# Kernel optimization log

Hardware: AMD Instinct MI355X
Metric: run time of the kernel (lower is better)

## Reference

```python
import jax, jax.numpy as jnp
import numpy as np

H = 16  # num_heads

def setup_inputs() -> dict:
    key = jax.random.key(0)
    ks = jax.random.split(key, 5)
    d = 1024
    s = 0.02
    return {
        'x': jax.random.normal(ks[0], (2, 2048, d), jnp.float32),
        'Wq': jax.random.normal(ks[1], (d, d), jnp.float32) * s,
        'bq': jnp.zeros((d,), jnp.float32),
        'Wk': jax.random.normal(ks[2], (d, d), jnp.float32) * s,
        'bk': jnp.zeros((d,), jnp.float32),
        'Wv': jax.random.normal(ks[3], (d, d), jnp.float32) * s,
        'bv': jnp.zeros((d,), jnp.float32),
        'Wo': jax.random.normal(ks[4], (d, d), jnp.float32) * s,
        'bo': jnp.zeros((d,), jnp.float32),
        'ln_scale': jnp.ones((d,), jnp.float32),
        'ln_bias': jnp.zeros((d,), jnp.float32),
    }

def _layernorm(x, scale, bias, eps=1e-6):
    mu = jnp.mean(x, axis=-1, keepdims=True)
    var = jnp.var(x, axis=-1, keepdims=True)
    return (x - mu) * jax.lax.rsqrt(var + eps) * scale + bias

def reference(x, Wq, bq, Wk, bk, Wv, bv, Wo, bo, ln_scale, ln_bias):
    b, n, d = x.shape
    hd = d // H
    scale = hd ** -0.5
    residual = x
    xn = _layernorm(x, ln_scale, ln_bias)
    # QKV projections, split heads: [b, n, d] -> [b, H, n, hd]
    def split(y):
        return y.reshape(b, n, H, hd).transpose(0, 2, 1, 3)
    q = split(xn @ Wq + bq)
    k = split(xn @ Wk + bk)
    v = split(xn @ Wv + bv)
    attn = jnp.einsum('bhid,bhjd->bhij', q, k) * scale
    attn = jax.nn.softmax(attn, axis=-1)
    out = jnp.einsum('bhij,bhjd->bhid', attn, v)
    out = out.transpose(0, 2, 1, 3).reshape(b, n, d)
    out = out @ Wo + bo
    return out + residual
```

## Files before the change

kernel.cpp:

```cpp
#include <hip/hip_runtime.h>

typedef __bf16 bf16;
typedef __bf16 bf16x8 __attribute__((ext_vector_type(8)));
typedef float f32x4 __attribute__((ext_vector_type(4)));

#define D_MODEL 1024
#define SEQ 2048
#define NH 16
#define HD 64

#define GLD16(gp, lp) __builtin_amdgcn_global_load_lds( \
    (const __attribute__((address_space(1))) void*)(gp), \
    (__attribute__((address_space(3))) void*)(lp), 16, 0, 0)

__device__ __forceinline__ int sigi(int y) {
    return (y & 0x23) | ((y & 0x18) >> 1) | ((y & 0x04) << 2);
}

__global__ __launch_bounds__(256) void ln_kernel(const float* __restrict__ x,
        const float* __restrict__ g, const float* __restrict__ bta,
        bf16* __restrict__ xnb) {
    int tok = blockIdx.x;
    const float* xr = x + (size_t)tok * D_MODEL;
    float v[4];
    float s = 0.f, ss = 0.f;
#pragma unroll
    for (int j = 0; j < 4; ++j) {
        int idx = threadIdx.x + j * 256;
        float t = xr[idx];
        v[j] = t; s += t; ss += t * t;
    }
#pragma unroll
    for (int m = 32; m; m >>= 1) { s += __shfl_xor(s, m, 64); ss += __shfl_xor(ss, m, 64); }
    __shared__ float red_s[4], red_ss[4];
    int w = threadIdx.x >> 6;
    if ((threadIdx.x & 63) == 0) { red_s[w] = s; red_ss[w] = ss; }
    __syncthreads();
    s  = red_s[0] + red_s[1] + red_s[2] + red_s[3];
    ss = red_ss[0] + red_ss[1] + red_ss[2] + red_ss[3];
    float mu  = s * (1.f / D_MODEL);
    float var = ss * (1.f / D_MODEL) - mu * mu;
    float rstd = rsqrtf(var + 1e-6f);
    bf16* orow = xnb + (size_t)tok * D_MODEL;
#pragma unroll
    for (int j = 0; j < 4; ++j) {
        int idx = threadIdx.x + j * 256;
        float xn = (v[j] - mu) * rstd * g[idx] + bta[idx];
        orow[idx] = (bf16)xn;
    }
}

__global__ __launch_bounds__(256) void transpose_kernel(const float* __restrict__ W0,
        const float* __restrict__ W1, const float* __restrict__ W2,
        const float* __restrict__ W3, bf16* __restrict__ wt) {
    __shared__ float tile[32][33];
    int mat = blockIdx.z;
    const float* W = mat == 0 ? W0 : mat == 1 ? W1 : mat == 2 ? W2 : W3;
    bf16* dst = wt + (size_t)mat * D_MODEL * D_MODEL;
    int k0 = blockIdx.x * 32, n0 = blockIdx.y * 32;
    int tx = threadIdx.x & 31, ty0 = threadIdx.x >> 5;
#pragma unroll
    for (int r = 0; r < 4; ++r) {
        int ty = ty0 + r * 8;
        tile[ty][tx] = W[(size_t)(k0 + ty) * D_MODEL + n0 + tx];
    }
    __syncthreads();
#pragma unroll
    for (int r = 0; r < 4; ++r) {
        int ty = ty0 + r * 8;
        dst[(size_t)(n0 + ty) * D_MODEL + k0 + tx] = (bf16)tile[tx][ty];
    }
}

__global__ __launch_bounds__(256) void qkv_gemm(const bf16* __restrict__ A,
        const bf16* __restrict__ Bt, const float* __restrict__ bq,
        const float* __restrict__ bk, const float* __restrict__ bv,
        bf16* __restrict__ qo, bf16* __restrict__ ko, bf16* __restrict__ vto) {
    __shared__ __align__(16) bf16 As[128 * 32];
    __shared__ __align__(16) bf16 Bs[128 * 32];
    int m0 = blockIdx.x * 128, n0 = blockIdx.y * 128;
    int tid = threadIdx.x;
    int w = tid >> 6, l = tid & 63, lm = l & 15, lq = l >> 4;
    int wm = (w >> 1) * 64, wn = (w & 1) * 64;
    f32x4 acc[4][4] = {};
    const bf16* ag = A  + (size_t)(m0 + w * 32 + (l >> 2)) * D_MODEL + (l & 3) * 8;
    const bf16* bg = Bt + (size_t)(n0 + w * 32 + (l >> 2)) * D_MODEL + (l & 3) * 8;
    bf16* asd = &As[(w * 32) * 32];
    bf16* bsd = &Bs[(w * 32) * 32];
    for (int k0 = 0; k0 < D_MODEL; k0 += 32) {
        GLD16(ag,                asd);
        GLD16(ag + 16 * D_MODEL, asd + 16 * 32);
        GLD16(bg,                bsd);
        GLD16(bg + 16 * D_MODEL, bsd + 16 * 32);
        ag += 32; bg += 32;
        __syncthreads();
        bf16x8 af[4], bf_[4];
#pragma unroll
        for (int f = 0; f < 4; ++f) af[f]  = *(const bf16x8*)&As[(wm + f * 16 + lm) * 32 + lq * 8];
#pragma unroll
        for (int f = 0; f < 4; ++f) bf_[f] = *(const bf16x8*)&Bs[(wn + f * 16 + lm) * 32 + lq * 8];
#pragma unroll
        for (int fm = 0; fm < 4; ++fm)
#pragma unroll
            for (int fn = 0; fn < 4; ++fn)
                acc[fm][fn] = __builtin_amdgcn_mfma_f32_16x16x32_bf16(af[fm], bf_[fn], acc[fm][fn], 0, 0, 0);
        __syncthreads();
    }
#pragma unroll
    for (int fn = 0; fn < 4; ++fn) {
        int n_g = n0 + wn + fn * 16 + lm;
        int mat = n_g >> 10, within = n_g & 1023;
        int h = within >> 6, hdp = within & 63;
        float bias = mat == 0 ? bq[within] : mat == 1 ? bk[within] : bv[within];
#pragma unroll
        for (int fm = 0; fm < 4; ++fm) {
#pragma unroll
            for (int r = 0; r < 4; ++r) {
                int m_g = m0 + wm + fm * 16 + lq * 4 + r;
                int b_ = m_g >> 11, i = m_g & 2047;
                int bh = b_ * NH + h;
                float val = acc[fm][fn][r] + bias;
                if (mat == 0) {
                    qo[((size_t)bh * SEQ + i) * HD + hdp] = (bf16)(val * 0.180336888f);
                } else {
                    int jt = i >> 6, jl = i & 63;
                    if (mat == 1) {
                        int idx = sigi(jl);
                        int nt_ = idx >> 4, lm_ = idx & 15;
                        int kc_ = hdp >> 5, lq_ = (hdp >> 3) & 3, e_ = hdp & 7;
                        ko[(size_t)bh * SEQ * HD + (size_t)jt * 4096 +
                           (kc_ * 4 + nt_) * 512 + (lq_ * 16 + lm_) * 8 + e_] = (bf16)val;
                    } else {
                        int nt_ = hdp >> 4, lm_ = hdp & 15;
                        int kc_ = jl >> 5, lq_ = (jl >> 3) & 3, e_ = jl & 7;
                        vto[(size_t)bh * SEQ * HD + (size_t)jt * 4096 +
                            (kc_ * 4 + nt_) * 512 + (lq_ * 16 + lm_) * 8 + e_] = (bf16)val;
                    }
                }
            }
        }
    }
}

__global__ __launch_bounds__(256) void attn_kernel(const bf16* __restrict__ q,
        const bf16* __restrict__ k, const bf16* __restrict__ vt,
        bf16* __restrict__ aout) {
    int i0 = blockIdx.x * 128;
    int bh = blockIdx.y;
    int tid = threadIdx.x;
    int w = tid >> 6, l = tid & 63, lm = l & 15, lq = l >> 4;
    const bf16* qb = q  + (size_t)bh * SEQ * HD;
    const bf16* kp = k  + (size_t)bh * SEQ * HD + l * 8;
    const bf16* vp = vt + (size_t)bh * SEQ * HD + l * 8;

    bf16x8 qf[2][2];
#pragma unroll
    for (int mf = 0; mf < 2; ++mf)
#pragma unroll
        for (int kc = 0; kc < 2; ++kc)
            qf[mf][kc] = *(const bf16x8*)(qb + (size_t)(i0 + w * 32 + mf * 16 + lm) * HD + kc * 32 + lq * 8);

    bf16x8 kcur[2][4];
#pragma unroll
    for (int kc = 0; kc < 2; ++kc)
#pragma unroll
        for (int nt = 0; nt < 4; ++nt)
            kcur[kc][nt] = *(const bf16x8*)(kp + (kc * 4 + nt) * 512);
    kp += 4096;

    f32x4 o[2][4] = {};
    float l_acc[2] = {0.f, 0.f};

    for (int j0 = 0; j0 < SEQ; j0 += 64) {
        bf16x8 vcur[2][4];
#pragma unroll
        for (int kc = 0; kc < 2; ++kc)
#pragma unroll
            for (int nt = 0; nt < 4; ++nt)
                vcur[kc][nt] = *(const bf16x8*)(vp + (kc * 4 + nt) * 512);
        vp += 4096;
        bf16x8 knxt[2][4];
        if (j0 + 64 < SEQ) {
#pragma unroll
            for (int kc = 0; kc < 2; ++kc)
#pragma unroll
                for (int nt = 0; nt < 4; ++nt)
                    knxt[kc][nt] = *(const bf16x8*)(kp + (kc * 4 + nt) * 512);
            kp += 4096;
        }
        f32x4 s[2][4] = {};
#pragma unroll
        for (int kc = 0; kc < 2; ++kc)
#pragma unroll
            for (int nt = 0; nt < 4; ++nt) {
                s[0][nt] = __builtin_amdgcn_mfma_f32_16x16x32_bf16(kcur[kc][nt], qf[0][kc], s[0][nt], 0, 0, 0);
                s[1][nt] = __builtin_amdgcn_mfma_f32_16x16x32_bf16(kcur[kc][nt], qf[1][kc], s[1][nt], 0, 0, 0);
            }
#pragma unroll
        for (int mf = 0; mf < 2; ++mf) {
            float psum = 0.f;
#pragma unroll
            for (int nt = 0; nt < 4; ++nt)
#pragma unroll
                for (int r = 0; r < 4; ++r) {
                    float p = exp2f(s[mf][nt][r]);
                    s[mf][nt][r] = p; psum += p;
                }
            l_acc[mf] += psum;
        }
#pragma unroll
        for (int kc = 0; kc < 2; ++kc) {
            bf16x8 pf[2];
#pragma unroll
            for (int mf = 0; mf < 2; ++mf)
#pragma unroll
                for (int jj = 0; jj < 8; ++jj)
                    pf[mf][jj] = (bf16)s[mf][2 * kc + (jj >> 2)][jj & 3];
#pragma unroll
            for (int nt = 0; nt < 4; ++nt) {
                o[0][nt] = __builtin_amdgcn_mfma_f32_16x16x32_bf16(pf[0], vcur[kc][nt], o[0][nt], 0, 0, 0);
                o[1][nt] = __builtin_amdgcn_mfma_f32_16x16x32_bf16(pf[1], vcur[kc][nt], o[1][nt], 0, 0, 0);
            }
        }
#pragma unroll
        for (int kc = 0; kc < 2; ++kc)
#pragma unroll
            for (int nt = 0; nt < 4; ++nt)
                kcur[kc][nt] = knxt[kc][nt];
    }
    int b_ = bh >> 4, h = bh & 15;
#pragma unroll
    for (int mf = 0; mf < 2; ++mf) {
        l_acc[mf] += __shfl_xor(l_acc[mf], 16, 64);
        l_acc[mf] += __shfl_xor(l_acc[mf], 32, 64);
        float linv[4];
#pragma unroll
        for (int r = 0; r < 4; ++r)
            linv[r] = 1.f / __shfl(l_acc[mf], lq * 4 + r, 64);
#pragma unroll
        for (int nt = 0; nt < 4; ++nt) {
#pragma unroll
            for (int r = 0; r < 4; ++r) {
                int i = i0 + w * 32 + mf * 16 + lq * 4 + r;
                int tok = b_ * SEQ + i;
                aout[(size_t)tok * D_MODEL + h * HD + nt * 16 + lm] = (bf16)(o[mf][nt][r] * linv[r]);
            }
        }
    }
}

__global__ __launch_bounds__(256) void out_gemm(const bf16* __restrict__ A,
        const bf16* __restrict__ Bt, const float* __restrict__ bo,
        const float* __restrict__ resid, float* __restrict__ out) {
    __shared__ __align__(16) bf16 As[128 * 32];
    __shared__ __align__(16) bf16 Bs[128 * 32];
    int m0 = blockIdx.x * 128, n0 = blockIdx.y * 128;
    int tid = threadIdx.x;
    int w = tid >> 6, l = tid & 63, lm = l & 15, lq = l >> 4;
    int wm = (w >> 1) * 64, wn = (w & 1) * 64;
    f32x4 acc[4][4] = {};
    const bf16* ag = A  + (size_t)(m0 + w * 32 + (l >> 2)) * D_MODEL + (l & 3) * 8;
    const bf16* bg = Bt + (size_t)(n0 + w * 32 + (l >> 2)) * D_MODEL + (l & 3) * 8;
    bf16* asd = &As[(w * 32) * 32];
    bf16* bsd = &Bs[(w * 32) * 32];
    for (int k0 = 0; k0 < D_MODEL; k0 += 32) {
        GLD16(ag,                asd);
        GLD16(ag + 16 * D_MODEL, asd + 16 * 32);
        GLD16(bg,                bsd);
        GLD16(bg + 16 * D_MODEL, bsd + 16 * 32);
        ag += 32; bg += 32;
        __syncthreads();
        bf16x8 af[4], bf_[4];
#pragma unroll
        for (int f = 0; f < 4; ++f) af[f]  = *(const bf16x8*)&As[(wm + f * 16 + lm) * 32 + lq * 8];
#pragma unroll
        for (int f = 0; f < 4; ++f) bf_[f] = *(const bf16x8*)&Bs[(wn + f * 16 + lm) * 32 + lq * 8];
#pragma unroll
        for (int fm = 0; fm < 4; ++fm)
#pragma unroll
            for (int fn = 0; fn < 4; ++fn)
                acc[fm][fn] = __builtin_amdgcn_mfma_f32_16x16x32_bf16(af[fm], bf_[fn], acc[fm][fn], 0, 0, 0);
        __syncthreads();
    }
#pragma unroll
    for (int fn = 0; fn < 4; ++fn) {
        int n_g = n0 + wn + fn * 16 + lm;
        float bias = bo[n_g];
#pragma unroll
        for (int fm = 0; fm < 4; ++fm) {
#pragma unroll
            for (int r = 0; r < 4; ++r) {
                int m_g = m0 + wm + fm * 16 + lq * 4 + r;
                size_t idx = (size_t)m_g * D_MODEL + n_g;
                out[idx] = acc[fm][fn][r] + bias + resid[idx];
            }
        }
    }
}

extern "C" void kernel_launch(void* const* d_in, const int* in_sizes, int n_in,
                              void* d_out, int out_size, void* d_ws, size_t ws_size,
                              hipStream_t stream) {
    const float* x  = (const float*)d_in[0];
    const float* Wq = (const float*)d_in[1];
    const float* bq = (const float*)d_in[2];
    const float* Wk = (const float*)d_in[3];
    const float* bk = (const float*)d_in[4];
    const float* Wv = (const float*)d_in[5];
    const float* bv = (const float*)d_in[6];
    const float* Wo = (const float*)d_in[7];
    const float* bo = (const float*)d_in[8];
    const float* g  = (const float*)d_in[9];
    const float* bt = (const float*)d_in[10];
    (void)in_sizes; (void)n_in; (void)out_size; (void)ws_size;

    char* ws = (char*)d_ws;
    const size_t M8 = (size_t)8 << 20;
    bf16* xnb = (bf16*)(ws);
    bf16* wt  = (bf16*)(ws + M8);
    bf16* qb  = (bf16*)(ws + 2 * M8);
    bf16* kb  = (bf16*)(ws + 3 * M8);
    bf16* vtb = (bf16*)(ws + 4 * M8);
    bf16* ao  = xnb;
    float* out = (float*)d_out;

    ln_kernel<<<4096, 256, 0, stream>>>(x, g, bt, xnb);
    transpose_kernel<<<dim3(32, 32, 4), 256, 0, stream>>>(Wq, Wk, Wv, Wo, wt);
    qkv_gemm<<<dim3(32, 24), 256, 0, stream>>>(xnb, wt, bq, bk, bv, qb, kb, vtb);
    attn_kernel<<<dim3(16, 32), 256, 0, stream>>>(qb, kb, vtb, ao);
    out_gemm<<<dim3(32, 8), 256, 0, stream>>>(ao, wt + (size_t)3 * D_MODEL * D_MODEL, bo, x, out);
}
```

Baseline: 233.2 us.

## Use plain K/V-transposed layouts and XCD-aware block mapping in attention

Result: slower. 274.9 us (+17.9%).

```diff
diff --git a/kernel.cpp b/kernel.cpp
--- a/kernel.cpp
+++ b/kernel.cpp
@@ -13,8 +13,8 @@
     (const __attribute__((address_space(1))) void*)(gp), \
     (__attribute__((address_space(3))) void*)(lp), 16, 0, 0)
 
-__device__ __forceinline__ int sigi(int y) {
-    return (y & 0x23) | ((y & 0x18) >> 1) | ((y & 0x04) << 2);
+__device__ __forceinline__ int sigp(int r) {
+    return (r & 0x23) | ((r & 0x0C) << 1) | ((r & 0x10) >> 2);
 }
 
 __global__ __launch_bounds__(256) void ln_kernel(const float* __restrict__ x,
@@ -120,23 +120,9 @@
                 int b_ = m_g >> 11, i = m_g & 2047;
                 int bh = b_ * NH + h;
                 float val = acc[fm][fn][r] + bias;
-                if (mat == 0) {
-                    qo[((size_t)bh * SEQ + i) * HD + hdp] = (bf16)(val * 0.180336888f);
-                } else {
-                    int jt = i >> 6, jl = i & 63;
-                    if (mat == 1) {
-                        int idx = sigi(jl);
-                        int nt_ = idx >> 4, lm_ = idx & 15;
-                        int kc_ = hdp >> 5, lq_ = (hdp >> 3) & 3, e_ = hdp & 7;
-                        ko[(size_t)bh * SEQ * HD + (size_t)jt * 4096 +
-                           (kc_ * 4 + nt_) * 512 + (lq_ * 16 + lm_) * 8 + e_] = (bf16)val;
-                    } else {
-                        int nt_ = hdp >> 4, lm_ = hdp & 15;
-                        int kc_ = jl >> 5, lq_ = (jl >> 3) & 3, e_ = jl & 7;
-                        vto[(size_t)bh * SEQ * HD + (size_t)jt * 4096 +
-                            (kc_ * 4 + nt_) * 512 + (lq_ * 16 + lm_) * 8 + e_] = (bf16)val;
-                    }
-                }
+                if (mat == 0)      qo [((size_t)bh * SEQ + i) * HD + hdp] = (bf16)(val * 0.180336888f);
+                else if (mat == 1) ko [((size_t)bh * SEQ + i) * HD + hdp] = (bf16)val;
+                else               vto[((size_t)bh * HD + hdp) * SEQ + i] = (bf16)val;
             }
         }
     }
@@ -145,13 +131,16 @@
 __global__ __launch_bounds__(256) void attn_kernel(const bf16* __restrict__ q,
         const bf16* __restrict__ k, const bf16* __restrict__ vt,
         bf16* __restrict__ aout) {
-    int i0 = blockIdx.x * 128;
-    int bh = blockIdx.y;
+    int bid = blockIdx.x;
+    int xcd = bid & 7;
+    int idx = bid >> 3;
+    int bh  = xcd + 8 * (idx & 3);
+    int i0  = (idx >> 2) * 128;
     int tid = threadIdx.x;
     int w = tid >> 6, l = tid & 63, lm = l & 15, lq = l >> 4;
     const bf16* qb = q  + (size_t)bh * SEQ * HD;
-    const bf16* kp = k  + (size_t)bh * SEQ * HD + l * 8;
-    const bf16* vp = vt + (size_t)bh * SEQ * HD + l * 8;
+    const bf16* kb = k  + (size_t)bh * SEQ * HD;
+    const bf16* vb = vt + (size_t)bh * HD * SEQ;
 
     bf16x8 qf[2][2];
 #pragma unroll
@@ -160,13 +149,19 @@
         for (int kc = 0; kc < 2; ++kc)
             qf[mf][kc] = *(const bf16x8*)(qb + (size_t)(i0 + w * 32 + mf * 16 + lm) * HD + kc * 32 + lq * 8);
 
+    const bf16* kpt[4]; const bf16* vpt[4];
+#pragma unroll
+    for (int nt = 0; nt < 4; ++nt) {
+        kpt[nt] = kb + (size_t)sigp(nt * 16 + lm) * HD + lq * 8;
+        vpt[nt] = vb + (size_t)(nt * 16 + lm) * SEQ + lq * 8;
+    }
+
     bf16x8 kcur[2][4];
 #pragma unroll
     for (int kc = 0; kc < 2; ++kc)
 #pragma unroll
         for (int nt = 0; nt < 4; ++nt)
-            kcur[kc][nt] = *(const bf16x8*)(kp + (kc * 4 + nt) * 512);
-    kp += 4096;
+            kcur[kc][nt] = *(const bf16x8*)(kpt[nt] + kc * 32);
 
     f32x4 o[2][4] = {};
     float l_acc[2] = {0.f, 0.f};
@@ -177,16 +172,14 @@
         for (int kc = 0; kc < 2; ++kc)
 #pragma unroll
             for (int nt = 0; nt < 4; ++nt)
-                vcur[kc][nt] = *(const bf16x8*)(vp + (kc * 4 + nt) * 512);
-        vp += 4096;
+                vcur[kc][nt] = *(const bf16x8*)(vpt[nt] + j0 + kc * 32);
         bf16x8 knxt[2][4];
         if (j0 + 64 < SEQ) {
 #pragma unroll
             for (int kc = 0; kc < 2; ++kc)
 #pragma unroll
                 for (int nt = 0; nt < 4; ++nt)
-                    knxt[kc][nt] = *(const bf16x8*)(kp + (kc * 4 + nt) * 512);
-            kp += 4096;
+                    knxt[kc][nt] = *(const bf16x8*)(kpt[nt] + (size_t)(j0 + 64) * HD + kc * 32);
         }
         f32x4 s[2][4] = {};
 #pragma unroll
@@ -327,6 +320,6 @@
     ln_kernel<<<4096, 256, 0, stream>>>(x, g, bt, xnb);
     transpose_kernel<<<dim3(32, 32, 4), 256, 0, stream>>>(Wq, Wk, Wv, Wo, wt);
     qkv_gemm<<<dim3(32, 24), 256, 0, stream>>>(xnb, wt, bq, bk, bv, qb, kb, vtb);
-    attn_kernel<<<dim3(16, 32), 256, 0, stream>>>(qb, kb, vtb, ao);
+    attn_kernel<<<512, 256, 0, stream>>>(qb, kb, vtb, ao);
     out_gemm<<<dim3(32, 8), 256, 0, stream>>>(ao, wt + (size_t)3 * D_MODEL * D_MODEL, bo, x, out);
 }
```
